# Kernel optimization log

Measured on AMD Instinct MI355X. Metric: run time of the kernel, lower is better.

The kernel has to match this reference:

```python
import jax, jax.numpy as jnp
import numpy as np

N_NODES = 50000
N_EDGES = 600000
CHANNELS = 128
HEADS = 8


def setup_inputs() -> dict:
    key = jax.random.key(0)
    k1, k2, k3 = jax.random.split(key, 3)
    x = jax.random.normal(k1, (N_NODES, CHANNELS), dtype=jnp.float32)
    edge_index = jax.random.randint(k2, (2, N_EDGES), 0, N_NODES, dtype=jnp.int32)
    att = jax.random.normal(k3, (HEADS, 2 * (CHANNELS // HEADS)), dtype=jnp.float32)
    return {"x": x, "edge_index": edge_index, "att": att}


def reference(x, edge_index, att):
    # x: [N, C], edge_index: [2, E], att: [H, 2*D] with D = C // H
    src, dst = edge_index[0], edge_index[1]
    n = x.shape[0]
    h = att.shape[0]
    d = att.shape[1] // 2

    x_src = x[src].reshape(-1, h, d)   # [E, H, D]
    x_dst = x[dst].reshape(-1, h, d)   # [E, H, D]

    # (cat([x_src, x_dst]) * att).sum(-1) == x_src @ att[:, :D] + x_dst @ att[:, D:]
    a_src, a_dst = att[:, :d], att[:, d:]
    alpha = jnp.einsum('ehd,hd->eh', x_src, a_src) + jnp.einsum('ehd,hd->eh', x_dst, a_dst)
    alpha = jnp.where(alpha >= 0, alpha, 0.2 * alpha)  # LeakyReLU(0.2)

    # segment softmax over dst; torch scatter_reduce amax includes the zero init,
    # so the per-node max is max(segment_max, 0)
    seg_max = jax.ops.segment_max(alpha, dst, num_segments=n)  # [N, H]
    seg_max = jnp.maximum(seg_max, 0.0)
    alpha = jnp.exp(alpha - seg_max[dst])
    seg_sum = jax.ops.segment_sum(alpha, dst, num_segments=n)  # [N, H]
    alpha = alpha / jnp.maximum(seg_sum[dst], 1e-10)

    # weighted scatter-add of source features
    weighted = x_src * alpha[..., None]                        # [E, H, D]
    out = jax.ops.segment_sum(weighted, dst, num_segments=n)   # [N, H, D]
    return out.reshape(n, -1)
```

## Files before the change

### kernel.cpp

```cpp
#include <hip/hip_runtime.h>

#define N_NODES  50000
#define N_EDGES  600000
#define CHANNELS 128
#define HEADS    8
#define HEAD_DIM 16
#define CAP      64

#define NBINS    256
#define CHUNK_E  1024
#define NCHUNK   ((N_EDGES + CHUNK_E - 1) / CHUNK_E)
#define SEGCAP   2816
#define NPB      200

#define LOGIT_VB ((N_NODES * (CHANNELS / 4)) / 256)
#define WPB      4

__global__ void hist_logit_kernel(const float* __restrict__ x,
                                  const float* __restrict__ att,
                                  const int*   __restrict__ dst,
                                  int*            __restrict__ hist,
                                  float*          __restrict__ ls8,
                                  float*          __restrict__ ld8,
                                  unsigned short* __restrict__ xb) {
    int b = blockIdx.x;
    int t = threadIdx.x;
    if (b < NCHUNK) {
        __shared__ int lh[NBINS];
        lh[t] = 0;
        __syncthreads();
        int base = b * CHUNK_E;
#pragma unroll
        for (int k = 0; k < 4; ++k) {
            int e = base + t + k * 256;
            if (e < N_EDGES) {
                unsigned bin = (unsigned)(dst[e] * NBINS) / N_NODES;
                atomicAdd(&lh[bin], 1);
            }
        }
        __syncthreads();
        hist[b * NBINS + t] = lh[t];
    } else {
        int gid = (b - NCHUNK) * 256 + t;
        int n  = gid >> 5;
        int c4 = gid & 31;
        int h  = c4 >> 2;
        int j4 = c4 & 3;

        float4 v = ((const float4*)x)[gid];

        unsigned int ux = __float_as_uint(v.x), uy = __float_as_uint(v.y);
        unsigned int uz = __float_as_uint(v.z), uw = __float_as_uint(v.w);
        ushort4 pk;
        pk.x = (unsigned short)((ux + 0x7FFFu + ((ux >> 16) & 1u)) >> 16);
        pk.y = (unsigned short)((uy + 0x7FFFu + ((uy >> 16) & 1u)) >> 16);
        pk.z = (unsigned short)((uz + 0x7FFFu + ((uz >> 16) & 1u)) >> 16);
        pk.w = (unsigned short)((uw + 0x7FFFu + ((uw >> 16) & 1u)) >> 16);
        ((ushort4*)xb)[gid] = pk;

        float4 as4 = ((const float4*)att)[h * 8 + j4];
        float4 ad4 = ((const float4*)att)[h * 8 + 4 + j4];
        float ts = v.x * as4.x + v.y * as4.y + v.z * as4.z + v.w * as4.w;
        float td = v.x * ad4.x + v.y * ad4.y + v.z * ad4.z + v.w * ad4.w;
        ts += __shfl_xor(ts, 1, 4); ts += __shfl_xor(ts, 2, 4);
        td += __shfl_xor(td, 1, 4); td += __shfl_xor(td, 2, 4);
        if (j4 == 0) {
            ls8[n * HEADS + h] = ts;
            ld8[n * HEADS + h] = td;
        }
    }
}

__global__ void scan_kernel(const int* __restrict__ hist,
                            int* __restrict__ offm,
                            int* __restrict__ bincnt) {
    __shared__ int lds[1024];
    int bin = blockIdx.x;
    int t = threadIdx.x;
    int v = (t < NCHUNK) ? hist[t * NBINS + bin] : 0;
    lds[t] = v;
    __syncthreads();
    for (int off = 1; off < 1024; off <<= 1) {
        int u = (t >= off) ? lds[t - off] : 0;
        __syncthreads();
        lds[t] += u;
        __syncthreads();
    }
    if (t < NCHUNK) offm[t * NBINS + bin] = lds[t] - v;
    if (t == 1023) bincnt[bin] = lds[t];
}

__global__ void binscatter_kernel(const int* __restrict__ src,
                                  const int* __restrict__ dst,
                                  const int* __restrict__ offm,
                                  unsigned*  __restrict__ ebuf) {
    __shared__ int loff[NBINS];
    __shared__ int lcnt[NBINS];
    int b = blockIdx.x;
    int t = threadIdx.x;
    loff[t] = offm[b * NBINS + t];
    lcnt[t] = 0;
    __syncthreads();
    int base = b * CHUNK_E;
#pragma unroll
    for (int k = 0; k < 4; ++k) {
        int e = base + t + k * 256;
        if (e < N_EDGES) {
            int d = dst[e];
            int s = src[e];
            unsigned bin = (unsigned)(d * NBINS) / N_NODES;
            int r = atomicAdd(&lcnt[bin], 1) + loff[bin];
            if (r < SEGCAP)
                ebuf[(size_t)bin * SEGCAP + r] = (unsigned)s | ((unsigned)d << 16);
        }
    }
}

__global__ void bucket_kernel(const unsigned* __restrict__ ebuf,
                              const int*      __restrict__ bincnt,
                              int*            __restrict__ cursor,
                              unsigned short* __restrict__ bucket) {
    __shared__ int lcnt[NPB];
    int b = blockIdx.x;
    int t = threadIdx.x;
    int n0 = (b * N_NODES + NBINS - 1) / NBINS;
    int n1 = ((b + 1) * N_NODES + NBINS - 1) / NBINS;
    int nn = n1 - n0;
    if (t < NPB) lcnt[t] = 0;
    __syncthreads();
    int cnt = min(bincnt[b], SEGCAP);
    for (int i = t; i < cnt; i += 256) {
        unsigned rec = ebuf[(size_t)b * SEGCAP + i];
        int s = (int)(rec & 0xFFFFu);
        int d = (int)(rec >> 16);
        int pos = atomicAdd(&lcnt[d - n0], 1);
        if (pos < CAP) bucket[(size_t)d * CAP + pos] = (unsigned short)s;
    }
    __syncthreads();
    if (t < nn) cursor[n0 + t] = lcnt[t];
}

__global__ void fused_gat_kernel(const unsigned short* __restrict__ xb,
                                 const float* __restrict__ ls8,
                                 const float* __restrict__ ld8,
                                 const int*   __restrict__ cursor,
                                 const unsigned short* __restrict__ bucket,
                                 float*       __restrict__ out) {
    __shared__ float s_p[WPB * CAP * HEADS];

    int wave = threadIdx.x >> 6;
    int lane = threadIdx.x & 63;
    int n = blockIdx.x * WPB + wave;
    if (n >= N_NODES) return;
    int h = lane >> 3;
    int j = lane & 7;
    int r   = lane >> 5;
    int l32 = lane & 31;
    int h2  = l32 >> 2;

    int   cnt_raw = cursor[n];
    int   myidx   = (int)bucket[(size_t)n * CAP + lane];
    float ldst    = ld8[n * HEADS + h];
    int cnt = (cnt_raw > CAP) ? CAP : cnt_raw;

    float* sp = s_p + wave * (CAP * HEADS);

    float av[8];
    float mymax = -1e30f;
#pragma unroll
    for (int k = 0; k < 8; ++k) {
        int i = j + 8 * k;
        av[k] = -1e30f;
        if (i < cnt) {
            int   s  = __shfl(myidx, i);
            float lg = ls8[s * HEADS + h] + ldst;
            float a  = (lg >= 0.0f) ? lg : 0.2f * lg;
            av[k] = a;
            mymax = fmaxf(mymax, a);
        }
    }
#pragma unroll
    for (int o = 4; o >= 1; o >>= 1) mymax = fmaxf(mymax, __shfl_xor(mymax, o, 8));
    float m = fmaxf(mymax, 0.0f);

    float myl = 0.0f;
#pragma unroll
    for (int k = 0; k < 8; ++k) {
        int i = j + 8 * k;
        if (i < cnt) {
            float p = __expf(av[k] - m);
            sp[i * HEADS + h] = p;
            myl += p;
        }
    }
#pragma unroll
    for (int o = 4; o >= 1; o >>= 1) myl += __shfl_xor(myl, o, 8);

#define LP(k) ( ((const uint2*)(xb + (size_t)__shfl(myidx, ((2*(k)+r) < cnt) ? (2*(k)+r) : 0) * CHANNELS))[l32] )
    uint2 q[8];
#pragma unroll
    for (int k = 0; k < 8; ++k) q[k] = LP(k);

    float a0 = 0.f, a1 = 0.f, a2 = 0.f, a3 = 0.f;
    int npair = (cnt + 1) >> 1;
    int k = 0;
    for (; k + 4 <= npair; k += 4) {
#pragma unroll
        for (int u = 0; u < 4; ++u) {
            int e2 = 2 * (k + u) + r;
            float p = (e2 < cnt) ? sp[e2 * HEADS + h2] : 0.0f;
            uint2 qq = q[u];
            a0 += p * __uint_as_float(qq.x << 16);
            a1 += p * __uint_as_float(qq.x & 0xFFFF0000u);
            a2 += p * __uint_as_float(qq.y << 16);
            a3 += p * __uint_as_float(qq.y & 0xFFFF0000u);
        }
#pragma unroll
        for (int u = 0; u < 4; ++u) q[u] = q[u + 4];
#pragma unroll
        for (int u = 0; u < 4; ++u) q[u + 4] = LP(k + 8 + u);
    }
    for (; k < npair; ++k) {
        int e2 = 2 * k + r;
        float p = (e2 < cnt) ? sp[e2 * HEADS + h2] : 0.0f;
        uint2 qq = q[0];
        a0 += p * __uint_as_float(qq.x << 16);
        a1 += p * __uint_as_float(qq.x & 0xFFFF0000u);
        a2 += p * __uint_as_float(qq.y << 16);
        a3 += p * __uint_as_float(qq.y & 0xFFFF0000u);
#pragma unroll
        for (int u = 0; u < 7; ++u) q[u] = q[u + 1];
    }
#undef LP

    a0 += __shfl_xor(a0, 32);
    a1 += __shfl_xor(a1, 32);
    a2 += __shfl_xor(a2, 32);
    a3 += __shfl_xor(a3, 32);

    float denom = __shfl(myl, h2 * 8);
    float inv = 1.0f / fmaxf(denom, 1e-10f);

    if (lane < 32) {
        float4 o4 = make_float4(a0 * inv, a1 * inv, a2 * inv, a3 * inv);
        ((float4*)(out + (size_t)n * CHANNELS))[l32] = o4;
    }
}

extern "C" void kernel_launch(void* const* d_in, const int* in_sizes, int n_in,
                              void* d_out, int out_size, void* d_ws, size_t ws_size,
                              hipStream_t stream) {
    const float* x   = (const float*)d_in[0];
    const int*   ei  = (const int*)  d_in[1];
    const float* att = (const float*)d_in[2];
    const int* src = ei;
    const int* dst = ei + N_EDGES;
    float* out = (float*)d_out;

    int*            hist   = (int*)d_ws;
    int*            offm   = hist + (size_t)NCHUNK * NBINS;
    int*            bincnt = offm + (size_t)NCHUNK * NBINS;
    unsigned*       ebuf   = (unsigned*)(bincnt + NBINS);
    int*            cursor = (int*)(ebuf + (size_t)NBINS * SEGCAP);
    unsigned short* bucket = (unsigned short*)(cursor + N_NODES);
    float*          ls8    = (float*)(bucket + (size_t)N_NODES * CAP);
    float*          ld8    = ls8 + (size_t)N_NODES * HEADS;
    unsigned short* xb     = (unsigned short*)(ld8 + (size_t)N_NODES * HEADS);

    hist_logit_kernel<<<NCHUNK + LOGIT_VB, 256, 0, stream>>>(
        x, att, dst, hist, ls8, ld8, xb);
    scan_kernel<<<NBINS, 1024, 0, stream>>>(hist, offm, bincnt);
    binscatter_kernel<<<NCHUNK, 256, 0, stream>>>(src, dst, offm, ebuf);
    bucket_kernel<<<NBINS, 256, 0, stream>>>(ebuf, bincnt, cursor, bucket);
    fused_gat_kernel<<<(N_NODES + WPB - 1) / WPB, 64 * WPB, 0, stream>>>(
        xb, ls8, ld8, cursor, bucket, out);
}
```

Baseline: 138.5 us.

## Transpose histogram, stage buckets in LDS, widen gather to 16-byte loads

Histogram is stored bin-major so the scan kernel reads contiguous counts, using 256 threads with three chunks each instead of a 1024-thread scan. The bucket kernel builds per-node rows in shared memory and writes them out with coalesced 16-byte stores instead of scattered 2-byte global writes. The aggregation kernel gathers four edges per wave step with uint4 loads (16 lanes per row) and eight accumulators, replacing the two-edge uint2 pipeline. It needs an extra shuffle reduction level and a large LDS buffer in the bucket kernel, which may limit occupancy there.

New measurement: 228.5 us. +65.0%, slower.

```diff
diff --git a/kernel.cpp b/kernel.cpp
--- a/kernel.cpp
+++ b/kernel.cpp
@@ -39,7 +39,7 @@
             }
         }
         __syncthreads();
-        hist[b * NBINS + t] = lh[t];
+        hist[t * NCHUNK + b] = lh[t];
     } else {
         int gid = (b - NCHUNK) * 256 + t;
         int n  = gid >> 5;
@@ -74,20 +74,27 @@
 __global__ void scan_kernel(const int* __restrict__ hist,
                             int* __restrict__ offm,
                             int* __restrict__ bincnt) {
-    __shared__ int lds[1024];
+    __shared__ int lds[256];
     int bin = blockIdx.x;
     int t = threadIdx.x;
-    int v = (t < NCHUNK) ? hist[t * NBINS + bin] : 0;
-    lds[t] = v;
-    __syncthreads();
-    for (int off = 1; off < 1024; off <<= 1) {
+    int c0 = t, c1 = t + 256, c2 = t + 512;
+    int v0 = hist[bin * NCHUNK + c0];
+    int v1 = (c1 < NCHUNK) ? hist[bin * NCHUNK + c1] : 0;
+    int v2 = (c2 < NCHUNK) ? hist[bin * NCHUNK + c2] : 0;
+    int s = v0 + v1 + v2;
+    lds[t] = s;
+    __syncthreads();
+    for (int off = 1; off < 256; off <<= 1) {
         int u = (t >= off) ? lds[t - off] : 0;
         __syncthreads();
         lds[t] += u;
         __syncthreads();
     }
-    if (t < NCHUNK) offm[t * NBINS + bin] = lds[t] - v;
-    if (t == 1023) bincnt[bin] = lds[t];
+    int base = lds[t] - s;
+    offm[c0 * NBINS + bin] = base;
+    if (c1 < NCHUNK) offm[c1 * NBINS + bin] = base + v0;
+    if (c2 < NCHUNK) offm[c2 * NBINS + bin] = base + v0 + v1;
+    if (t == 255) bincnt[bin] = lds[255];
 }
 
 __global__ void binscatter_kernel(const int* __restrict__ src,
@@ -120,6 +127,7 @@
                               const int*      __restrict__ bincnt,
                               int*            __restrict__ cursor,
                               unsigned short* __restrict__ bucket) {
+    __shared__ unsigned short rows[NPB * CAP];
     __shared__ int lcnt[NPB];
     int b = blockIdx.x;
     int t = threadIdx.x;
@@ -134,9 +142,13 @@
         int s = (int)(rec & 0xFFFFu);
         int d = (int)(rec >> 16);
         int pos = atomicAdd(&lcnt[d - n0], 1);
-        if (pos < CAP) bucket[(size_t)d * CAP + pos] = (unsigned short)s;
-    }
-    __syncthreads();
+        if (pos < CAP) rows[(d - n0) * CAP + pos] = (unsigned short)s;
+    }
+    __syncthreads();
+    int nq = nn * (CAP * 2 / 16);
+    uint4* gdst = (uint4*)(bucket + (size_t)n0 * CAP);
+    const uint4* lsrc = (const uint4*)rows;
+    for (int i = t; i < nq; i += 256) gdst[i] = lsrc[i];
     if (t < nn) cursor[n0 + t] = lcnt[t];
 }
 
@@ -154,9 +166,9 @@
     if (n >= N_NODES) return;
     int h = lane >> 3;
     int j = lane & 7;
-    int r   = lane >> 5;
-    int l32 = lane & 31;
-    int h2  = l32 >> 2;
+    int r2  = lane >> 4;
+    int l16 = lane & 15;
+    int h3  = l16 >> 1;
 
     int   cnt_raw = cursor[n];
     int   myidx   = (int)bucket[(size_t)n * CAP + lane];
@@ -196,54 +208,45 @@
 #pragma unroll
     for (int o = 4; o >= 1; o >>= 1) myl += __shfl_xor(myl, o, 8);
 
-#define LP(k) ( ((const uint2*)(xb + (size_t)__shfl(myidx, ((2*(k)+r) < cnt) ? (2*(k)+r) : 0) * CHANNELS))[l32] )
-    uint2 q[8];
-#pragma unroll
-    for (int k = 0; k < 8; ++k) q[k] = LP(k);
-
-    float a0 = 0.f, a1 = 0.f, a2 = 0.f, a3 = 0.f;
-    int npair = (cnt + 1) >> 1;
-    int k = 0;
-    for (; k + 4 <= npair; k += 4) {
-#pragma unroll
-        for (int u = 0; u < 4; ++u) {
-            int e2 = 2 * (k + u) + r;
-            float p = (e2 < cnt) ? sp[e2 * HEADS + h2] : 0.0f;
-            uint2 qq = q[u];
-            a0 += p * __uint_as_float(qq.x << 16);
-            a1 += p * __uint_as_float(qq.x & 0xFFFF0000u);
-            a2 += p * __uint_as_float(qq.y << 16);
-            a3 += p * __uint_as_float(qq.y & 0xFFFF0000u);
-        }
-#pragma unroll
-        for (int u = 0; u < 4; ++u) q[u] = q[u + 4];
-#pragma unroll
-        for (int u = 0; u < 4; ++u) q[u + 4] = LP(k + 8 + u);
-    }
-    for (; k < npair; ++k) {
-        int e2 = 2 * k + r;
-        float p = (e2 < cnt) ? sp[e2 * HEADS + h2] : 0.0f;
-        uint2 qq = q[0];
+#define LQ4(k) ( ((const uint4*)(xb + (size_t)__shfl(myidx, ((4*(k)+r2) < cnt) ? (4*(k)+r2) : 0) * CHANNELS))[l16] )
+    uint4 q[4];
+#pragma unroll
+    for (int k = 0; k < 4; ++k) q[k] = LQ4(k);
+
+    float a0=0.f,a1=0.f,a2=0.f,a3=0.f,a4=0.f,a5=0.f,a6=0.f,a7=0.f;
+    int nquad = (cnt + 3) >> 2;
+    for (int k = 0; k < nquad; ++k) {
+        uint4 qq = q[k & 3];
+        q[k & 3] = LQ4(k + 4);
+        int e = 4 * k + r2;
+        float p = (e < cnt) ? sp[e * HEADS + h3] : 0.0f;
         a0 += p * __uint_as_float(qq.x << 16);
         a1 += p * __uint_as_float(qq.x & 0xFFFF0000u);
         a2 += p * __uint_as_float(qq.y << 16);
         a3 += p * __uint_as_float(qq.y & 0xFFFF0000u);
-#pragma unroll
-        for (int u = 0; u < 7; ++u) q[u] = q[u + 1];
-    }
-#undef LP
-
-    a0 += __shfl_xor(a0, 32);
-    a1 += __shfl_xor(a1, 32);
-    a2 += __shfl_xor(a2, 32);
-    a3 += __shfl_xor(a3, 32);
-
-    float denom = __shfl(myl, h2 * 8);
+        a4 += p * __uint_as_float(qq.z << 16);
+        a5 += p * __uint_as_float(qq.z & 0xFFFF0000u);
+        a6 += p * __uint_as_float(qq.w << 16);
+        a7 += p * __uint_as_float(qq.w & 0xFFFF0000u);
+    }
+#undef LQ4
+
+    a0 += __shfl_xor(a0, 16); a0 += __shfl_xor(a0, 32);
+    a1 += __shfl_xor(a1, 16); a1 += __shfl_xor(a1, 32);
+    a2 += __shfl_xor(a2, 16); a2 += __shfl_xor(a2, 32);
+    a3 += __shfl_xor(a3, 16); a3 += __shfl_xor(a3, 32);
+    a4 += __shfl_xor(a4, 16); a4 += __shfl_xor(a4, 32);
+    a5 += __shfl_xor(a5, 16); a5 += __shfl_xor(a5, 32);
+    a6 += __shfl_xor(a6, 16); a6 += __shfl_xor(a6, 32);
+    a7 += __shfl_xor(a7, 16); a7 += __shfl_xor(a7, 32);
+
+    float denom = __shfl(myl, h3 * 8);
     float inv = 1.0f / fmaxf(denom, 1e-10f);
 
-    if (lane < 32) {
-        float4 o4 = make_float4(a0 * inv, a1 * inv, a2 * inv, a3 * inv);
-        ((float4*)(out + (size_t)n * CHANNELS))[l32] = o4;
+    if (lane < 16) {
+        float4* op = (float4*)(out + (size_t)n * CHANNELS + l16 * 8);
+        op[0] = make_float4(a0 * inv, a1 * inv, a2 * inv, a3 * inv);
+        op[1] = make_float4(a4 * inv, a5 * inv, a6 * inv, a7 * inv);
     }
 }
 
@@ -258,7 +261,7 @@
     float* out = (float*)d_out;
 
     int*            hist   = (int*)d_ws;
-    int*            offm   = hist + (size_t)NCHUNK * NBINS;
+    int*            offm   = hist + (size_t)NBINS * NCHUNK;
     int*            bincnt = offm + (size_t)NCHUNK * NBINS;
     unsigned*       ebuf   = (unsigned*)(bincnt + NBINS);
     int*            cursor = (int*)(ebuf + (size_t)NBINS * SEGCAP);
@@ -269,7 +272,7 @@
 
     hist_logit_kernel<<<NCHUNK + LOGIT_VB, 256, 0, stream>>>(
         x, att, dst, hist, ls8, ld8, xb);
-    scan_kernel<<<NBINS, 1024, 0, stream>>>(hist, offm, bincnt);
+    scan_kernel<<<NBINS, 256, 0, stream>>>(hist, offm, bincnt);
     binscatter_kernel<<<NCHUNK, 256, 0, stream>>>(src, dst, offm, ebuf);
     bucket_kernel<<<NBINS, 256, 0, stream>>>(ebuf, bincnt, cursor, bucket);
     fused_gat_kernel<<<(N_NODES + WPB - 1) / WPB, 64 * WPB, 0, stream>>>(
```
